# Optimization experiments

Measured on AMD Instinct MI355X. Metric: run time of the kernel, lower is better.

The kernel has to match this reference:

```python
import jax, jax.numpy as jnp
import numpy as np

B, N, D, H, O, A, L = 128, 100, 2048, 1024, 1600, 400, 2048


def _mlp(x, w1, b1, w2, b2, w3, b3):
    h = jax.nn.relu(x @ w1 + b1)
    h = jax.nn.relu(h @ w2 + b2)
    return jax.nn.softmax(h @ w3 + b3, axis=2)  # softmax over class dim (dim=2)


def setup_inputs() -> dict:
    key = jax.random.key(0)
    ks = jax.random.split(key, 18)

    def lin(kw, fan_in, fan_out):
        s = 1.0 / np.sqrt(fan_in)
        return jax.random.normal(kw, (fan_in, fan_out), jnp.float32) * s

    x = jax.random.normal(ks[0], (B, N, D), jnp.float32)
    num_descs = jax.random.randint(ks[1], (B,), 0, N, jnp.int32)
    label_img = jnp.sort(jax.random.randint(ks[2], (L,), 0, B, jnp.int32))
    obj_labels = jax.random.randint(ks[3], (L,), 0, O)
    att_labels = jax.random.randint(ks[4], (L,), 0, A)

    inp = dict(x=x, num_descs=num_descs, label_img=label_img,
               obj_labels=obj_labels, att_labels=att_labels,
               w1o=lin(ks[5], D, H), b1o=jnp.zeros((H,), jnp.float32),
               w2o=lin(ks[6], H, H), b2o=jnp.zeros((H,), jnp.float32),
               w3o=lin(ks[7], H, O), b3o=jnp.zeros((O,), jnp.float32),
               w1a=lin(ks[8], D, H), b1a=jnp.zeros((H,), jnp.float32),
               w2a=lin(ks[9], H, H), b2a=jnp.zeros((H,), jnp.float32),
               w3a=lin(ks[10], H, A), b3a=jnp.zeros((A,), jnp.float32))
    return inp


def reference(x, num_descs, label_img, obj_labels, att_labels,
              w1o, b1o, w2o, b2o, w3o, b3o,
              w1a, b1a, w2a, b2a, w3a, b3a):
    po = _mlp(x, w1o, b1o, w2o, b2o, w3o, b3o)  # [B, N, O]
    pa = _mlp(x, w1a, b1a, w2a, b2a, w3a, b3a)  # [B, N, A]

    rows = jnp.arange(po.shape[1])  # [N]
    # per-label gather of the prob column for its object/attribute class -> [L, N]
    p_obj = po[label_img[:, None], rows[None, :], obj_labels[:, None]]
    p_att = pa[label_img[:, None], rows[None, :], att_labels[:, None]]
    # ragged unpad (descs beyond num_descs[img] excluded from argmax)
    valid = rows[None, :] < num_descs[label_img][:, None]
    score = jnp.where(valid, p_obj * p_att, -jnp.inf)
    desc = jnp.argmax(score, axis=1)  # [L]

    obj_dists = po[label_img, desc, :]  # [L, O]
    att_dists = pa[label_img, desc, :]  # [L, A]
    return (obj_dists, att_dists)
```

## Files before the change

kernel.cpp:

```cpp
#include <hip/hip_runtime.h>
#include <hip/hip_bf16.h>
#include <math.h>

#define Bq 128
#define Nq 100
#define Dq 2048
#define Hq 1024
#define Oq 1600
#define Aq 400
#define Lq 2048
#define Mq (Bq * Nq)
#define OqP 1664
#define AqP 512

typedef __attribute__((ext_vector_type(8))) short bf16x8;
typedef __attribute__((ext_vector_type(16))) float f32x16;
typedef unsigned short ushort;


__device__ __forceinline__ void split1(float v, ushort& h, ushort& l) {
    __hip_bfloat16 bh = __float2bfloat16(v);
    float fh = __bfloat162float(bh);
    __hip_bfloat16 bl = __float2bfloat16(v - fh);
    h = __builtin_bit_cast(ushort, bh);
    l = __builtin_bit_cast(ushort, bl);
}

__device__ __forceinline__ void gl_lds16(const ushort* g, ushort* lds) {
    __builtin_amdgcn_global_load_lds(
        (const __attribute__((address_space(1))) unsigned int*)g,
        (__attribute__((address_space(3))) unsigned int*)lds,
        16, 0, 0);
}

__global__ void build_offsets(const int* __restrict__ num_descs,
                              int* __restrict__ off, int* __restrict__ mc,
                              int* __restrict__ rowmap)
{
    __shared__ int cnt[Bq];
    __shared__ int offs[Bq + 1];
    const int t = threadIdx.x;
    int nd = num_descs[t];
    nd = nd < 0 ? 0 : (nd > Nq ? Nq : nd);
    const int c = nd < 1 ? 1 : nd;
    cnt[t] = c;
    __syncthreads();
    if (t == 0) {
        int s = 0;
        for (int i = 0; i < Bq; i++) { offs[i] = s; s += cnt[i]; }
        offs[Bq] = s;
        mc[0] = s;
        mc[1] = (s + 127) & ~127;
        mc[2] = (s + 255) & ~(int)255;
    }
    __syncthreads();
    off[t] = offs[t];
    for (int i = t; i < Mq; i += Bq) rowmap[i] = -1;
    __syncthreads();
    const int o = offs[t];
    for (int n = 0; n < c; n++) rowmap[o + n] = t * Nq + n;
}

__global__ __launch_bounds__(256) void split_compact(const float* __restrict__ x,
                              const int* __restrict__ rowmap,
                              const int* __restrict__ mc,
                              ushort* __restrict__ hi, ushort* __restrict__ lo)
{
    const int KB = Dq / 16;
    const int nbc = Dq / 64;
    const int rt = blockIdx.x / nbc;
    const int bc = (blockIdx.x - rt * nbc) * 64;
    if (rt * 32 >= mc[2]) return;

    __shared__ float t[32][66];
    const int tid = threadIdx.x;
    {
        const int row = tid >> 3;
        const int coff = (tid & 7) * 8;
        const int crow = rt * 32 + row;
        const int orig = (crow < mc[0]) ? rowmap[crow] : -1;
        float v[8];
        if (orig < 0) {
#pragma unroll
            for (int e = 0; e < 8; e++) v[e] = 0.f;
        } else {
            const float* src = x + (size_t)orig * Dq + bc + coff;
            float4 v0 = *(const float4*)(src);
            float4 v1 = *(const float4*)(src + 4);
            v[0] = v0.x; v[1] = v0.y; v[2] = v0.z; v[3] = v0.w;
            v[4] = v1.x; v[5] = v1.y; v[6] = v1.z; v[7] = v1.w;
        }
#pragma unroll
        for (int e = 0; e < 8; e++) t[row][coff + e] = v[e];
    }
    __syncthreads();

    const int wave = tid >> 6;
    const int lane = tid & 63;
    const int r32 = lane & 31;
    const int cl = wave * 16 + (lane >> 5) * 8;
    ushort h[8], l[8];
#pragma unroll
    for (int e = 0; e < 8; e++) split1(t[r32][cl + e], h[e], l[e]);
    const size_t wid = (size_t)rt * KB + (bc >> 4) + wave;
    const size_t a = wid * 512 + (size_t)lane * 8;
    *(bf16x8*)(hi + a) = *(bf16x8*)h;
    *(bf16x8*)(lo + a) = *(bf16x8*)l;
}

struct TSeg { const float* W; ushort* Th; ushort* Tl; int K; int N; int gx; int base; };
struct TSegs { TSeg s[6]; };

__global__ void tsplit_all(TSegs a)
{
    const int id = blockIdx.x;
    TSeg sg = a.s[5];
#pragma unroll
    for (int i = 4; i >= 0; i--) if (id < a.s[i + 1].base) sg = a.s[i];
    const int local = id - sg.base;
    const int bn = (local % sg.gx) * 32;
    const int bk = (local / sg.gx) * 32;
    const int KB = sg.K >> 4;

    __shared__ float t[32][33];
    const int tx = threadIdx.x & 31, ty = threadIdx.x >> 5;
#pragma unroll
    for (int i = 0; i < 4; i++) {
        const int k = bk + ty + i * 8, n = bn + tx;
        t[ty + i * 8][tx] = (n < sg.N) ? sg.W[(size_t)k * sg.N + n] : 0.f;
    }
    __syncthreads();

    const int wave = threadIdx.x >> 6;
    const int lane = threadIdx.x & 63;
    const int kc = wave & 1;
    const int hl = wave >> 1;
    const int nloc = lane & 31;
    const int kloc = kc * 16 + (lane >> 5) * 8;
    ushort v8[8];
#pragma unroll
    for (int e = 0; e < 8; e++) {
        ushort h, l;
        split1(t[kloc + e][nloc], h, l);
        v8[e] = hl ? l : h;
    }
    const size_t chunk = (size_t)((bn >> 5)) * KB + (bk >> 4) + kc;
    ushort* dst = (hl ? sg.Tl : sg.Th) + chunk * 512 + (size_t)lane * 8;
    *(bf16x8*)dst = *(bf16x8*)v8;
}

struct GArgs {
    const ushort* Ah; const ushort* Al;
    const ushort* Bh; const ushort* Bl;
    const float* bias;
    float* Cf; ushort* Ch; ushort* Cl;
    int K, Npad, Nreal, ldc, mode;
};

__global__ __launch_bounds__(256, 2) void gemm_split(GArgs g0, GArgs g1,
                                                     const int* __restrict__ mcp,
                                                     int nct0, int nct)
{
    const int ny = mcp[2] >> 8;
    const int nact = nct * ny;
    const int hw = blockIdx.x;
    if (hw >= nact) return;
    const int q = nact >> 3, r = nact & 7, xcd = hw & 7, pos = hw >> 3;
    const int L = (xcd < r ? xcd * (q + 1) : r * (q + 1) + (xcd - r) * q) + pos;
    const int by = L / nct;
    const int ct = L - by * nct;

    const GArgs g = (ct < nct0) ? g0 : g1;
    const int bm = by * 256;
    const int bn = (ct < nct0 ? ct : ct - nct0) * 128;

    const int KB = g.K >> 4;

    __shared__ __align__(16) ushort sAh[12288];
    __shared__ __align__(16) ushort sAl[12288];
    __shared__ __align__(16) ushort sBh[6144];
    __shared__ __align__(16) ushort sBl[6144];

    const int tid  = threadIdx.x;
    const int wave = tid >> 6;
    const int lane = tid & 63;
    const int wm = wave >> 1;
    const int wn = wave & 1;
    const int l31  = lane & 31;
    const int half = lane >> 5;

    const ushort* gAh0 = g.Ah + ((size_t)(bm / 32 + wave) * KB) * 512 + lane * 8;
    const ushort* gAh1 = g.Ah + ((size_t)(bm / 32 + wave + 4) * KB) * 512 + lane * 8;
    const ushort* gAl0 = g.Al + ((size_t)(bm / 32 + wave) * KB) * 512 + lane * 8;
    const ushort* gAl1 = g.Al + ((size_t)(bm / 32 + wave + 4) * KB) * 512 + lane * 8;
    const ushort* gBh  = g.Bh + ((size_t)(bn / 32 + wave) * KB) * 512 + lane * 8;
    const ushort* gBl  = g.Bl + ((size_t)(bn / 32 + wave) * KB) * 512 + lane * 8;

    f32x16 acc[4][2] = {};

    auto STAGE = [&](int c) {
        const size_t go = (size_t)c * 512;
        const int sa = (c % 3) * 4096;
        const int sb = (c % 3) * 2048;
        gl_lds16(gAh0 + go, &sAh[sa + (wave << 9)]);
        gl_lds16(gAh1 + go, &sAh[sa + ((wave + 4) << 9)]);
        gl_lds16(gAl0 + go, &sAl[sa + (wave << 9)]);
        gl_lds16(gAl1 + go, &sAl[sa + ((wave + 4) << 9)]);
        gl_lds16(gBh + go, &sBh[sb + (wave << 9)]);
        gl_lds16(gBl + go, &sBl[sb + (wave << 9)]);
    };

    auto PHASE = [&](int c, int stage_c, int drain) {
        const int sa = (c % 3) * 4096;
        const int sb = (c % 3) * 2048;
        bf16x8 ah[4], al[4], bh[2], bl[2];
#pragma unroll
        for (int i = 0; i < 4; i++) {
            const int o = sa + (wm * 4 + i) * 512 + lane * 8;
            ah[i] = *(const bf16x8*)&sAh[o];
            al[i] = *(const bf16x8*)&sAl[o];
        }
#pragma unroll
        for (int j = 0; j < 2; j++) {
            const int o = sb + (wn * 2 + j) * 512 + lane * 8;
            bh[j] = *(const bf16x8*)&sBh[o];
            bl[j] = *(const bf16x8*)&sBl[o];
        }
        if (stage_c >= 0) STAGE(stage_c);
        __builtin_amdgcn_s_setprio(1);
#pragma unroll
        for (int i = 0; i < 4; i++)
#pragma unroll
            for (int j = 0; j < 2; j++) {
                acc[i][j] = __builtin_amdgcn_mfma_f32_32x32x16_bf16(ah[i], bh[j], acc[i][j], 0, 0, 0);
                acc[i][j] = __builtin_amdgcn_mfma_f32_32x32x16_bf16(ah[i], bl[j], acc[i][j], 0, 0, 0);
                acc[i][j] = __builtin_amdgcn_mfma_f32_32x32x16_bf16(al[i], bh[j], acc[i][j], 0, 0, 0);
            }
        __builtin_amdgcn_s_setprio(0);
        if (drain == 6)      asm volatile("s_waitcnt vmcnt(6)" ::: "memory");
        else if (drain == 0) asm volatile("s_waitcnt vmcnt(0)" ::: "memory");
        if (drain >= 0) {
            asm volatile("s_waitcnt lgkmcnt(0)" ::: "memory");
            asm volatile("s_barrier" ::: "memory");
        }
    };

    STAGE(0); STAGE(1);
    asm volatile("s_waitcnt vmcnt(6)" ::: "memory");
    asm volatile("s_barrier" ::: "memory");

    for (int c = 0; c < KB - 2; ++c) PHASE(c, c + 2, 6);
    PHASE(KB - 2, -1, 0);
    PHASE(KB - 1, -1, -1);

    const int KC = g.ldc >> 4;
#pragma unroll
    for (int j = 0; j < 2; j++) {
        const int col = bn + (wn * 2 + j) * 32 + l31;
        if (col < g.Nreal) {
            const float bv = g.bias[col];
#pragma unroll
            for (int i = 0; i < 4; i++) {
#pragma unroll
                for (int r = 0; r < 16; r++) {
                    const int row = bm + (wm * 4 + i) * 32 + (r & 3) + 8 * (r >> 2) + 4 * half;
                    float v = acc[i][j][r] + bv;
                    if (g.mode == 1) {
                        v = fmaxf(v, 0.f);
                        ushort h, l;
                        split1(v, h, l);
                        const size_t chunk = (size_t)(row >> 5) * KC + (col >> 4);
                        const size_t adr = chunk * 512
                            + (size_t)((row & 31) + 32 * ((col >> 3) & 1)) * 8 + (col & 7);
                        g.Ch[adr] = h;
                        g.Cl[adr] = l;
                    } else {
                        g.Cf[(size_t)row * g.ldc + col] = v;
                    }
                }
            }
        }
    }
}

__global__ void softmax_stats2(const float* __restrict__ Zo, const float* __restrict__ Za,
                               const int* __restrict__ mc,
                               float* __restrict__ mxo, float* __restrict__ smo,
                               float* __restrict__ mxa, float* __restrict__ sma)
{
    const int r = blockIdx.x;
    if (r >= mc[0]) return;
    __shared__ float red[256];
    const int t = threadIdx.x;
#pragma unroll
    for (int br = 0; br < 2; br++) {
        const float* Z = br ? Za : Zo;
        const int ncols = br ? Aq : Oq;
        float* mx = br ? mxa : mxo;
        float* sm = br ? sma : smo;
        const float4* row = (const float4*)(Z + (size_t)r * ncols);
        const int n4 = ncols >> 2;
        float m = -INFINITY;
        for (int c = t; c < n4; c += 256) {
            const float4 v = row[c];
            m = fmaxf(m, fmaxf(fmaxf(v.x, v.y), fmaxf(v.z, v.w)));
        }
        red[t] = m;
        __syncthreads();
        for (int s = 128; s > 0; s >>= 1) {
            if (t < s) red[t] = fmaxf(red[t], red[t + s]);
            __syncthreads();
        }
        m = red[0];
        __syncthreads();
        float su = 0.f;
        for (int c = t; c < n4; c += 256) {
            const float4 v = row[c];
            su += expf(v.x - m) + expf(v.y - m) + expf(v.z - m) + expf(v.w - m);
        }
        red[t] = su;
        __syncthreads();
        for (int s = 128; s > 0; s >>= 1) {
            if (t < s) red[t] += red[t + s];
            __syncthreads();
        }
        if (t == 0) { mx[r] = m; sm[r] = red[0]; }
        __syncthreads();
    }
}

__global__ void argmax_gather(
    const float* __restrict__ Zo, const float* __restrict__ Za,
    const float* __restrict__ mxo, const float* __restrict__ smo,
    const float* __restrict__ mxa, const float* __restrict__ sma,
    const int* __restrict__ label_img, const int* __restrict__ num_descs,
    const int* __restrict__ obj_labels, const int* __restrict__ att_labels,
    const int* __restrict__ off, float* __restrict__ out)
{
    const int l = blockIdx.x;
    const int b = label_img[l];
    const int nd = num_descs[b];
    const int r0 = off[b];
    const int t = threadIdx.x;

    __shared__ float ss[128];
    __shared__ int   si[128];
    if (t < 128) {
        float score = -INFINITY;
        if (t < Nq && t < nd) {
            const int r = r0 + t;
            const float po = expf(Zo[(size_t)r * Oq + obj_labels[l]] - mxo[r]) / smo[r];
            const float pa = expf(Za[(size_t)r * Aq + att_labels[l]] - mxa[r]) / sma[r];
            score = po * pa;
        }
        ss[t] = score;
        si[t] = t;
    }
    __syncthreads();
    for (int s = 64; s > 0; s >>= 1) {
        if (t < s) {
            const float s2 = ss[t + s];
            const int   i2 = si[t + s];
            if (s2 > ss[t] || (s2 == ss[t] && i2 < si[t])) { ss[t] = s2; si[t] = i2; }
        }
        __syncthreads();
    }
    const int r = r0 + si[0];

    {
        const float mo = mxo[r];
        const float iso = 1.0f / smo[r];
        const float4* zo4 = (const float4*)(Zo + (size_t)r * Oq);
        float4* oo4 = (float4*)(out + (size_t)l * Oq);
        for (int c = t; c < (Oq >> 2); c += 256) {
            const float4 v = zo4[c];
            float4 w;
            w.x = expf(v.x - mo) * iso;
            w.y = expf(v.y - mo) * iso;
            w.z = expf(v.z - mo) * iso;
            w.w = expf(v.w - mo) * iso;
            oo4[c] = w;
        }
    }
    {
        const float ma = mxa[r];
        const float isa = 1.0f / sma[r];
        const float4* za4 = (const float4*)(Za + (size_t)r * Aq);
        float4* oa4 = (float4*)(out + (size_t)Lq * Oq + (size_t)l * Aq);
        for (int c = t; c < (Aq >> 2); c += 256) {
            const float4 v = za4[c];
            float4 w;
            w.x = expf(v.x - ma) * isa;
            w.y = expf(v.y - ma) * isa;
            w.z = expf(v.z - ma) * isa;
            w.w = expf(v.w - ma) * isa;
            oa4[c] = w;
        }
    }
}

extern "C" void kernel_launch(void* const* d_in, const int* in_sizes, int n_in,
                              void* d_out, int out_size, void* d_ws, size_t ws_size,
                              hipStream_t stream)
{
    const float* x          = (const float*)d_in[0];
    const int*   num_descs  = (const int*)d_in[1];
    const int*   label_img  = (const int*)d_in[2];
    const int*   obj_labels = (const int*)d_in[3];
    const int*   att_labels = (const int*)d_in[4];
    const float* w1o = (const float*)d_in[5];  const float* b1o = (const float*)d_in[6];
    const float* w2o = (const float*)d_in[7];  const float* b2o = (const float*)d_in[8];
    const float* w3o = (const float*)d_in[9];  const float* b3o = (const float*)d_in[10];
    const float* w1a = (const float*)d_in[11]; const float* b1a = (const float*)d_in[12];
    const float* w2a = (const float*)d_in[13]; const float* b2a = (const float*)d_in[14];
    const float* w3a = (const float*)d_in[15]; const float* b3a = (const float*)d_in[16];
    float* out = (float*)d_out;

    char* p = (char*)d_ws;
    auto carve = [&](size_t bytes) { char* q = p; p += (bytes + 255) & ~(size_t)255; return q; };

    char* bufA = carve((size_t)Mq * Dq * 2 * 2);
    char* bufB = carve((size_t)Mq * Hq * 2 * 2 * 2);
    ushort* w1oth = (ushort*)carve((size_t)Hq * Dq * 2);  ushort* w1otl = (ushort*)carve((size_t)Hq * Dq * 2);
    ushort* w1ath = (ushort*)carve((size_t)Hq * Dq * 2);  ushort* w1atl = (ushort*)carve((size_t)Hq * Dq * 2);
    ushort* w2oth = (ushort*)carve((size_t)Hq * Hq * 2);  ushort* w2otl = (ushort*)carve((size_t)Hq * Hq * 2);
    ushort* w2ath = (ushort*)carve((size_t)Hq * Hq * 2);  ushort* w2atl = (ushort*)carve((size_t)Hq * Hq * 2);
    ushort* w3oth = (ushort*)carve((size_t)OqP * Hq * 2); ushort* w3otl = (ushort*)carve((size_t)OqP * Hq * 2);
    ushort* w3ath = (ushort*)carve((size_t)AqP * Hq * 2); ushort* w3atl = (ushort*)carve((size_t)AqP * Hq * 2);
    float* mxo = (float*)carve(Mq * 4); float* smo = (float*)carve(Mq * 4);
    float* mxa = (float*)carve(Mq * 4); float* sma = (float*)carve(Mq * 4);
    int* off    = (int*)carve(Bq * 4);
    int* mc     = (int*)carve(4 * 4);
    int* rowmap = (int*)carve(Mq * 4);

    ushort* xh = (ushort*)bufA;
    ushort* xl = xh + (size_t)Mq * Dq;
    ushort* h2oh = (ushort*)bufA;
    ushort* h2ol = h2oh + (size_t)Mq * Hq;
    ushort* h2ah = h2ol + (size_t)Mq * Hq;
    ushort* h2al = h2ah + (size_t)Mq * Hq;
    ushort* h1oh = (ushort*)bufB;
    ushort* h1ol = h1oh + (size_t)Mq * Hq;
    ushort* h1ah = h1ol + (size_t)Mq * Hq;
    ushort* h1al = h1ah + (size_t)Mq * Hq;
    float* z3o = (float*)bufB;
    float* z3a = z3o + (size_t)Mq * Oq;

    build_offsets<<<1, 128, 0, stream>>>(num_descs, off, mc, rowmap);
    split_compact<<<(Mq / 32) * (Dq / 64), 256, 0, stream>>>(x, rowmap, mc, xh, xl);

    {
        TSegs ts;
        int base = 0;
        auto seg = [&](const float* W, ushort* Th, ushort* Tl, int K, int N, int Npad) {
            TSeg s; s.W = W; s.Th = Th; s.Tl = Tl; s.K = K; s.N = N;
            s.gx = Npad / 32; s.base = base; base += (Npad / 32) * (K / 32); return s;
        };
        ts.s[0] = seg(w1o, w1oth, w1otl, Dq, Hq, Hq);
        ts.s[1] = seg(w1a, w1ath, w1atl, Dq, Hq, Hq);
        ts.s[2] = seg(w2o, w2oth, w2otl, Hq, Hq, Hq);
        ts.s[3] = seg(w2a, w2ath, w2atl, Hq, Hq, Hq);
        ts.s[4] = seg(w3o, w3oth, w3otl, Hq, Oq, OqP);
        ts.s[5] = seg(w3a, w3ath, w3atl, Hq, Aq, AqP);
        tsplit_all<<<base, 256, 0, stream>>>(ts);
    }

    {
        GArgs go = { xh, xl, w1oth, w1otl, b1o, nullptr, h1oh, h1ol, Dq, Hq, Hq, Hq, 1 };
        GArgs ga = { xh, xl, w1ath, w1atl, b1a, nullptr, h1ah, h1al, Dq, Hq, Hq, Hq, 1 };
        gemm_split<<<16 * (Mq / 256), 256, 0, stream>>>(go, ga, mc, 8, 16);
    }
    {
        GArgs go = { h1oh, h1ol, w2oth, w2otl, b2o, nullptr, h2oh, h2ol, Hq, Hq, Hq, Hq, 1 };
        GArgs ga = { h1ah, h1al, w2ath, w2atl, b2a, nullptr, h2ah, h2al, Hq, Hq, Hq, Hq, 1 };
        gemm_split<<<16 * (Mq / 256), 256, 0, stream>>>(go, ga, mc, 8, 16);
    }
    {
        GArgs go = { h2oh, h2ol, w3oth, w3otl, b3o, z3o, nullptr, nullptr, Hq, OqP, Oq, Oq, 0 };
        GArgs ga = { h2ah, h2al, w3ath, w3atl, b3a, z3a, nullptr, nullptr, Hq, AqP, Aq, Aq, 0 };
        gemm_split<<<(OqP / 128 + AqP / 128) * (Mq / 256), 256, 0, stream>>>(go, ga, mc,
                                                                            OqP / 128,
                                                                            OqP / 128 + AqP / 128);
    }

    softmax_stats2<<<Mq, 256, 0, stream>>>(z3o, z3a, mc, mxo, smo, mxa, sma);
    argmax_gather<<<Lq, 256, 0, stream>>>(z3o, z3a, mxo, smo, mxa, sma,
                                          label_img, num_descs, obj_labels, att_labels, off, out);
}
```

Before: 544.4 us.

## Make split GEMM persistent with an atomic tile counter

Turns gemm_split into a persistent kernel. A fixed grid of 512 blocks repeatedly grabs tile indices from a global atomic counter, which build_offsets resets before each run. This drops the static XCD-aware block-to-tile remap and the early exit of surplus blocks, aiming for dynamic load balancing over the data-dependent number of active row tiles. In exchange it adds an atomic plus a barrier per tile. Tiles are also no longer grouped per XCD, which can hurt L2 reuse.

```diff
diff --git a/kernel.cpp b/kernel.cpp
--- a/kernel.cpp
+++ b/kernel.cpp
@@ -35,11 +35,12 @@
 
 __global__ void build_offsets(const int* __restrict__ num_descs,
                               int* __restrict__ off, int* __restrict__ mc,
-                              int* __restrict__ rowmap)
+                              int* __restrict__ rowmap, int* __restrict__ ctr)
 {
     __shared__ int cnt[Bq];
     __shared__ int offs[Bq + 1];
     const int t = threadIdx.x;
+    if (t < 3) ctr[t] = 0;
     int nd = num_descs[t];
     nd = nd < 0 ? 0 : (nd > Nq ? Nq : nd);
     const int c = nd < 1 ? 1 : nd;
@@ -159,27 +160,17 @@
 
 __global__ __launch_bounds__(256, 2) void gemm_split(GArgs g0, GArgs g1,
                                                      const int* __restrict__ mcp,
-                                                     int nct0, int nct)
+                                                     int nct0, int nct,
+                                                     int* __restrict__ ctr)
 {
     const int ny = mcp[2] >> 8;
     const int nact = nct * ny;
-    const int hw = blockIdx.x;
-    if (hw >= nact) return;
-    const int q = nact >> 3, r = nact & 7, xcd = hw & 7, pos = hw >> 3;
-    const int L = (xcd < r ? xcd * (q + 1) : r * (q + 1) + (xcd - r) * q) + pos;
-    const int by = L / nct;
-    const int ct = L - by * nct;
-
-    const GArgs g = (ct < nct0) ? g0 : g1;
-    const int bm = by * 256;
-    const int bn = (ct < nct0 ? ct : ct - nct0) * 128;
-
-    const int KB = g.K >> 4;
 
     __shared__ __align__(16) ushort sAh[12288];
     __shared__ __align__(16) ushort sAl[12288];
     __shared__ __align__(16) ushort sBh[6144];
     __shared__ __align__(16) ushort sBl[6144];
+    __shared__ int s_idx;
 
     const int tid  = threadIdx.x;
     const int wave = tid >> 6;
@@ -189,93 +180,107 @@
     const int l31  = lane & 31;
     const int half = lane >> 5;
 
-    const ushort* gAh0 = g.Ah + ((size_t)(bm / 32 + wave) * KB) * 512 + lane * 8;
-    const ushort* gAh1 = g.Ah + ((size_t)(bm / 32 + wave + 4) * KB) * 512 + lane * 8;
-    const ushort* gAl0 = g.Al + ((size_t)(bm / 32 + wave) * KB) * 512 + lane * 8;
-    const ushort* gAl1 = g.Al + ((size_t)(bm / 32 + wave + 4) * KB) * 512 + lane * 8;
-    const ushort* gBh  = g.Bh + ((size_t)(bn / 32 + wave) * KB) * 512 + lane * 8;
-    const ushort* gBl  = g.Bl + ((size_t)(bn / 32 + wave) * KB) * 512 + lane * 8;
-
-    f32x16 acc[4][2] = {};
-
-    auto STAGE = [&](int c) {
-        const size_t go = (size_t)c * 512;
-        const int sa = (c % 3) * 4096;
-        const int sb = (c % 3) * 2048;
-        gl_lds16(gAh0 + go, &sAh[sa + (wave << 9)]);
-        gl_lds16(gAh1 + go, &sAh[sa + ((wave + 4) << 9)]);
-        gl_lds16(gAl0 + go, &sAl[sa + (wave << 9)]);
-        gl_lds16(gAl1 + go, &sAl[sa + ((wave + 4) << 9)]);
-        gl_lds16(gBh + go, &sBh[sb + (wave << 9)]);
-        gl_lds16(gBl + go, &sBl[sb + (wave << 9)]);
-    };
-
-    auto PHASE = [&](int c, int stage_c, int drain) {
-        const int sa = (c % 3) * 4096;
-        const int sb = (c % 3) * 2048;
-        bf16x8 ah[4], al[4], bh[2], bl[2];
-#pragma unroll
-        for (int i = 0; i < 4; i++) {
-            const int o = sa + (wm * 4 + i) * 512 + lane * 8;
-            ah[i] = *(const bf16x8*)&sAh[o];
-            al[i] = *(const bf16x8*)&sAl[o];
-        }
+    for (;;) {
+        if (tid == 0) s_idx = atomicAdd(ctr, 1);
+        __syncthreads();
+        const int idx = s_idx;
+        if (idx >= nact) return;
+        const int by = idx / nct;
+        const int ct = idx - by * nct;
+
+        const GArgs g = (ct < nct0) ? g0 : g1;
+        const int bm = by * 256;
+        const int bn = (ct < nct0 ? ct : ct - nct0) * 128;
+        const int KB = g.K >> 4;
+
+        const ushort* gAh0 = g.Ah + ((size_t)(bm / 32 + wave) * KB) * 512 + lane * 8;
+        const ushort* gAh1 = g.Ah + ((size_t)(bm / 32 + wave + 4) * KB) * 512 + lane * 8;
+        const ushort* gAl0 = g.Al + ((size_t)(bm / 32 + wave) * KB) * 512 + lane * 8;
+        const ushort* gAl1 = g.Al + ((size_t)(bm / 32 + wave + 4) * KB) * 512 + lane * 8;
+        const ushort* gBh  = g.Bh + ((size_t)(bn / 32 + wave) * KB) * 512 + lane * 8;
+        const ushort* gBl  = g.Bl + ((size_t)(bn / 32 + wave) * KB) * 512 + lane * 8;
+
+        f32x16 acc[4][2] = {};
+
+        auto STAGE = [&](int c) {
+            const size_t go = (size_t)c * 512;
+            const int sa = (c % 3) * 4096;
+            const int sb = (c % 3) * 2048;
+            gl_lds16(gAh0 + go, &sAh[sa + (wave << 9)]);
+            gl_lds16(gAh1 + go, &sAh[sa + ((wave + 4) << 9)]);
+            gl_lds16(gAl0 + go, &sAl[sa + (wave << 9)]);
+            gl_lds16(gAl1 + go, &sAl[sa + ((wave + 4) << 9)]);
+            gl_lds16(gBh + go, &sBh[sb + (wave << 9)]);
+            gl_lds16(gBl + go, &sBl[sb + (wave << 9)]);
+        };
+
+        auto PHASE = [&](int c, int stage_c, int drain) {
+            const int sa = (c % 3) * 4096;
+            const int sb = (c % 3) * 2048;
+            bf16x8 ah[4], al[4], bh[2], bl[2];
+#pragma unroll
+            for (int i = 0; i < 4; i++) {
+                const int o = sa + (wm * 4 + i) * 512 + lane * 8;
+                ah[i] = *(const bf16x8*)&sAh[o];
+                al[i] = *(const bf16x8*)&sAl[o];
+            }
+#pragma unroll
+            for (int j = 0; j < 2; j++) {
+                const int o = sb + (wn * 2 + j) * 512 + lane * 8;
+                bh[j] = *(const bf16x8*)&sBh[o];
+                bl[j] = *(const bf16x8*)&sBl[o];
+            }
+            if (stage_c >= 0) STAGE(stage_c);
+            __builtin_amdgcn_s_setprio(1);
+#pragma unroll
+            for (int i = 0; i < 4; i++)
+#pragma unroll
+                for (int j = 0; j < 2; j++) {
+                    acc[i][j] = __builtin_amdgcn_mfma_f32_32x32x16_bf16(ah[i], bh[j], acc[i][j], 0, 0, 0);
+                    acc[i][j] = __builtin_amdgcn_mfma_f32_32x32x16_bf16(ah[i], bl[j], acc[i][j], 0, 0, 0);
+                    acc[i][j] = __builtin_amdgcn_mfma_f32_32x32x16_bf16(al[i], bh[j], acc[i][j], 0, 0, 0);
+                }
+            __builtin_amdgcn_s_setprio(0);
+            if (drain == 6)      asm volatile("s_waitcnt vmcnt(6)" ::: "memory");
+            else if (drain == 0) asm volatile("s_waitcnt vmcnt(0)" ::: "memory");
+            if (drain >= 0) {
+                asm volatile("s_waitcnt lgkmcnt(0)" ::: "memory");
+                asm volatile("s_barrier" ::: "memory");
+            }
+        };
+
+        STAGE(0); STAGE(1);
+        asm volatile("s_waitcnt vmcnt(6)" ::: "memory");
+        asm volatile("s_barrier" ::: "memory");
+
+        for (int c = 0; c < KB - 2; ++c) PHASE(c, c + 2, 6);
+        PHASE(KB - 2, -1, 0);
+        PHASE(KB - 1, -1, -1);
+
+        const int KC = g.ldc >> 4;
 #pragma unroll
         for (int j = 0; j < 2; j++) {
-            const int o = sb + (wn * 2 + j) * 512 + lane * 8;
-            bh[j] = *(const bf16x8*)&sBh[o];
-            bl[j] = *(const bf16x8*)&sBl[o];
-        }
-        if (stage_c >= 0) STAGE(stage_c);
-        __builtin_amdgcn_s_setprio(1);
-#pragma unroll
-        for (int i = 0; i < 4; i++)
-#pragma unroll
-            for (int j = 0; j < 2; j++) {
-                acc[i][j] = __builtin_amdgcn_mfma_f32_32x32x16_bf16(ah[i], bh[j], acc[i][j], 0, 0, 0);
-                acc[i][j] = __builtin_amdgcn_mfma_f32_32x32x16_bf16(ah[i], bl[j], acc[i][j], 0, 0, 0);
-                acc[i][j] = __builtin_amdgcn_mfma_f32_32x32x16_bf16(al[i], bh[j], acc[i][j], 0, 0, 0);
-            }
-        __builtin_amdgcn_s_setprio(0);
-        if (drain == 6)      asm volatile("s_waitcnt vmcnt(6)" ::: "memory");
-        else if (drain == 0) asm volatile("s_waitcnt vmcnt(0)" ::: "memory");
-        if (drain >= 0) {
-            asm volatile("s_waitcnt lgkmcnt(0)" ::: "memory");
-            asm volatile("s_barrier" ::: "memory");
-        }
-    };
-
-    STAGE(0); STAGE(1);
-    asm volatile("s_waitcnt vmcnt(6)" ::: "memory");
-    asm volatile("s_barrier" ::: "memory");
-
-    for (int c = 0; c < KB - 2; ++c) PHASE(c, c + 2, 6);
-    PHASE(KB - 2, -1, 0);
-    PHASE(KB - 1, -1, -1);
-
-    const int KC = g.ldc >> 4;
-#pragma unroll
-    for (int j = 0; j < 2; j++) {
-        const int col = bn + (wn * 2 + j) * 32 + l31;
-        if (col < g.Nreal) {
-            const float bv = g.bias[col];
-#pragma unroll
-            for (int i = 0; i < 4; i++) {
-#pragma unroll
-                for (int r = 0; r < 16; r++) {
-                    const int row = bm + (wm * 4 + i) * 32 + (r & 3) + 8 * (r >> 2) + 4 * half;
-                    float v = acc[i][j][r] + bv;
-                    if (g.mode == 1) {
-                        v = fmaxf(v, 0.f);
-                        ushort h, l;
-                        split1(v, h, l);
-                        const size_t chunk = (size_t)(row >> 5) * KC + (col >> 4);
-                        const size_t adr = chunk * 512
-                            + (size_t)((row & 31) + 32 * ((col >> 3) & 1)) * 8 + (col & 7);
-                        g.Ch[adr] = h;
-                        g.Cl[adr] = l;
-                    } else {
-                        g.Cf[(size_t)row * g.ldc + col] = v;
+            const int col = bn + (wn * 2 + j) * 32 + l31;
+            if (col < g.Nreal) {
+                const float bv = g.bias[col];
+#pragma unroll
+                for (int i = 0; i < 4; i++) {
+#pragma unroll
+                    for (int r = 0; r < 16; r++) {
+                        const int row = bm + (wm * 4 + i) * 32 + (r & 3) + 8 * (r >> 2) + 4 * half;
+                        float v = acc[i][j][r] + bv;
+                        if (g.mode == 1) {
+                            v = fmaxf(v, 0.f);
+                            ushort h, l;
+                            split1(v, h, l);
+                            const size_t chunk = (size_t)(row >> 5) * KC + (col >> 4);
+                            const size_t adr = chunk * 512
+                                + (size_t)((row & 31) + 32 * ((col >> 3) & 1)) * 8 + (col & 7);
+                            g.Ch[adr] = h;
+                            g.Cl[adr] = l;
+                        } else {
+                            g.Cf[(size_t)row * g.ldc + col] = v;
+                        }
                     }
                 }
             }
@@ -432,6 +437,7 @@
     int* off    = (int*)carve(Bq * 4);
     int* mc     = (int*)carve(4 * 4);
     int* rowmap = (int*)carve(Mq * 4);
+    int* ctr    = (int*)carve(4 * 4);
 
     ushort* xh = (ushort*)bufA;
     ushort* xl = xh + (size_t)Mq * Dq;
@@ -446,7 +452,7 @@
     float* z3o = (float*)bufB;
     float* z3a = z3o + (size_t)Mq * Oq;
 
-    build_offsets<<<1, 128, 0, stream>>>(num_descs, off, mc, rowmap);
+    build_offsets<<<1, 128, 0, stream>>>(num_descs, off, mc, rowmap, ctr);
     split_compact<<<(Mq / 32) * (Dq / 64), 256, 0, stream>>>(x, rowmap, mc, xh, xl);
 
     {
@@ -468,19 +474,17 @@
     {
         GArgs go = { xh, xl, w1oth, w1otl, b1o, nullptr, h1oh, h1ol, Dq, Hq, Hq, Hq, 1 };
         GArgs ga = { xh, xl, w1ath, w1atl, b1a, nullptr, h1ah, h1al, Dq, Hq, Hq, Hq, 1 };
-        gemm_split<<<16 * (Mq / 256), 256, 0, stream>>>(go, ga, mc, 8, 16);
+        gemm_split<<<512, 256, 0, stream>>>(go, ga, mc, 8, 16, ctr + 0);
     }
     {
         GArgs go = { h1oh, h1ol, w2oth, w2otl, b2o, nullptr, h2oh, h2ol, Hq, Hq, Hq, Hq, 1 };
         GArgs ga = { h1ah, h1al, w2ath, w2atl, b2a, nullptr, h2ah, h2al, Hq, Hq, Hq, Hq, 1 };
-        gemm_split<<<16 * (Mq / 256), 256, 0, stream>>>(go, ga, mc, 8, 16);
+        gemm_split<<<512, 256, 0, stream>>>(go, ga, mc, 8, 16, ctr + 1);
     }
     {
         GArgs go = { h2oh, h2ol, w3oth, w3otl, b3o, z3o, nullptr, nullptr, Hq, OqP, Oq, Oq, 0 };
         GArgs ga = { h2ah, h2al, w3ath, w3atl, b3a, z3a, nullptr, nullptr, Hq, AqP, Aq, Aq, 0 };
-        gemm_split<<<(OqP / 128 + AqP / 128) * (Mq / 256), 256, 0, stream>>>(go, ga, mc,
-                                                                            OqP / 128,
-                                                                            OqP / 128 + AqP / 128);
+        gemm_split<<<512, 256, 0, stream>>>(go, ga, mc, OqP / 128, OqP / 128 + AqP / 128, ctr + 2);
     }
 
     softmax_stats2<<<Mq, 256, 0, stream>>>(z3o, z3a, mc, mxo, smo, mxa, sma);
```

Measured after the change: 587.7 us. 1.08x slower.
